# Optimization experiments

Measured on AMD Instinct MI355X. Metric: run time of the kernel, lower is better.

## Reference

```python
import jax, jax.numpy as jnp
import numpy as np

B, N = 2, 6
H, W = 64, 64            # BEV grid
FH, FW = 32, 88          # camera feature map
DIM, FEAT_DIM = 128, 128
HEADS, DH = 4, 32
QW1, QW2 = 8, 8          # query window
KW1, KW2 = 4, 11         # key/val window
IMG_H, IMG_W = 224, 480
EPS = 1e-5


def _ln(t, g, b):
    m = t.mean(-1, keepdims=True)
    v = ((t - m) ** 2).mean(-1, keepdims=True)
    return (t - m) / jnp.sqrt(v + EPS) * g + b


def _bn_relu_conv(t, g, b, Wc):
    # eval-mode BatchNorm2d (running_mean=0, running_var=1) -> ReLU -> 1x1 conv
    y = jax.nn.relu(t / jnp.sqrt(1.0 + EPS) * g[:, None, None] + b[:, None, None])
    return jnp.einsum('oc,nchw->nohw', Wc, y)


def _normalize(t, axis):
    n = jnp.sqrt(jnp.sum(t * t, axis=axis, keepdims=True))
    return t / jnp.maximum(n, 1e-12)


def _win(t, w1, w2):
    # (..., X*w1, Y*w2, d) -> (..., X, Y, w1, w2, d)
    s = t.shape
    t = t.reshape(*s[:-3], s[-3] // w1, w1, s[-2] // w2, w2, s[-1])
    return jnp.swapaxes(t, -4, -3)


def _unwin(t):
    # (..., X, Y, w1, w2, d) -> (..., X*w1, Y*w2, d)
    s = t.shape
    return jnp.swapaxes(t, -4, -3).reshape(*s[:-5], s[-5] * s[-3], s[-4] * s[-2], s[-1])


def _gridwin(t, w1, w2):
    bb, nn, Ht, Wt, d = t.shape
    t = t.reshape(bb, nn, w1, Ht // w1, w2, Wt // w2, d)
    return t.transpose(0, 1, 3, 5, 2, 4, 6)  # (b, n, X, Y, w1, w2, d)


def _cross_win_attn(qw, kw, vw, ln_g, ln_b, Wqkv, bqkv, Wp, bp, skip):
    b, n, X, Y, w1, w2, d = qw.shape
    f1, f2 = kw.shape[4], kw.shape[5]
    L = X * Y
    q = qw.transpose(0, 2, 3, 1, 4, 5, 6).reshape(b, L, n * w1 * w2, d)
    k = kw.transpose(0, 2, 3, 1, 4, 5, 6).reshape(b, L, n * f1 * f2, d)
    v = vw.transpose(0, 2, 3, 1, 4, 5, 6).reshape(b, L, n * f1 * f2, d)
    q = _ln(q, ln_g[0], ln_b[0]) @ Wqkv[0] + bqkv[0]
    k = _ln(k, ln_g[1], ln_b[1]) @ Wqkv[1] + bqkv[1]
    v = _ln(v, ln_g[2], ln_b[2]) @ Wqkv[2] + bqkv[2]
    split = lambda t: t.reshape(*t.shape[:-1], HEADS, DH)  # head-major channel split
    q, k, v = split(q), split(k), split(v)
    att = jax.nn.softmax(DH ** -0.5 * jnp.einsum('blqhd,blkhd->bhlqk', q, k), axis=-1)
    o = jnp.einsum('bhlqk,blkhd->blqhd', att, v).reshape(b, L, n * w1 * w2, HEADS * DH)
    o = o @ Wp + bp
    o = o.reshape(b, X, Y, n, w1, w2, d).mean(3)  # mean over cameras
    return o + skip


def _forward(x, grid, feature, I_inv, E_inv,
             bn_fl_g, bn_fl_b, W_fl, bn_fp_g, bn_fp_b, W_fp,
             W_bev, b_bev, W_img, W_cam,
             attn_ln_g, attn_ln_b, attn_Wqkv, attn_bqkv, attn_Wp, attn_bp,
             pn_g, pn_b, Wma, bma, Wmb, bmb, post_g, post_b):
    b, n = feature.shape[:2]
    # image plane (buffer)
    xs = jnp.linspace(0.0, 1.0, FW) * IMG_W
    ys = jnp.linspace(0.0, 1.0, FH) * IMG_H
    gx, gy = jnp.meshgrid(xs, ys)  # (FH, FW) each
    plane = jnp.stack([gx, gy, jnp.ones_like(gx)], 0).reshape(3, FH * FW)
    # camera embedding from translation column of E_inv
    c = E_inv[..., -1]                                   # (b, n, 4)
    c_embed = jnp.einsum('oc,bnc->bno', W_cam, c)        # (b, n, dim)
    # unprojected rays
    cam = jnp.einsum('bnij,jk->bnik', I_inv, plane)      # (b, n, 3, HW)
    cam = jnp.concatenate([cam, jnp.ones_like(cam[:, :, :1])], 2)
    d = jnp.einsum('bnij,bnjk->bnik', E_inv, cam)        # (b, n, 4, HW)
    d_img = d.reshape(b, n, 4, FH, FW)
    d_embed = jnp.einsum('oc,bnchw->bnohw', W_img, d_img)
    img_embed = _normalize(d_embed - c_embed[..., None, None], axis=2)
    # BEV positional embedding
    w_embed = jnp.einsum('oc,chw->ohw', W_bev, grid[:2]) + b_bev[:, None, None]
    bev_embed = _normalize(w_embed[None, None] - c_embed[..., None, None], axis=2)  # (b,n,dim,H,W)
    feat = feature.reshape(b * n, FEAT_DIM, FH, FW)
    key_im = img_embed + _bn_relu_conv(feat, bn_fp_g, bn_fp_b, W_fp).reshape(b, n, DIM, FH, FW)
    val_im = _bn_relu_conv(feat, bn_fl_g, bn_fl_b, W_fl).reshape(b, n, DIM, FH, FW)
    query = bev_embed + x[:, None]                       # (b, n, dim, H, W)
    # channel-last
    q_im = query.transpose(0, 1, 3, 4, 2)
    k_im = key_im.transpose(0, 1, 3, 4, 2)
    v_im = val_im.transpose(0, 1, 3, 4, 2)
    x_im = x.transpose(0, 2, 3, 1)
    # stage 1: local windows
    qw = _win(q_im, QW1, QW2)
    kw = _win(k_im, KW1, KW2)
    vw = _win(v_im, KW1, KW2)
    o1 = _cross_win_attn(qw, kw, vw, attn_ln_g[0], attn_ln_b[0], attn_Wqkv[0],
                         attn_bqkv[0], attn_Wp[0], attn_bp[0], _win(x_im, QW1, QW2))
    q1 = _unwin(o1)                                      # (b, H, W, d)
    q1 = q1 + jax.nn.gelu(_ln(q1, pn_g[0], pn_b[0]) @ Wma[0] + bma[0], approximate=False) @ Wmb[0] + bmb[0]
    # stage 2: grid (swapped) windows
    qg = jnp.broadcast_to(q1[:, None], (b, n) + q1.shape[1:])
    o2 = _cross_win_attn(_win(qg, QW1, QW2), _gridwin(k_im, KW1, KW2), _gridwin(v_im, KW1, KW2),
                         attn_ln_g[1], attn_ln_b[1], attn_Wqkv[1], attn_bqkv[1],
                         attn_Wp[1], attn_bp[1], _win(q1, QW1, QW2))
    q2 = _unwin(o2)
    q2 = q2 + jax.nn.gelu(_ln(q2, pn_g[1], pn_b[1]) @ Wma[1] + bma[1], approximate=False) @ Wmb[1] + bmb[1]
    out = _ln(q2, post_g, post_b)
    return out.transpose(0, 3, 1, 2)                     # (b, dim, H, W)


def setup_inputs() -> dict:
    key = jax.random.key(0)
    ks = jax.random.split(key, 16)
    rn = lambda i, shape, sc=0.02: jax.random.normal(ks[i], shape, dtype=jnp.float32) * sc
    return {
        'index': 0,
        'x': jax.random.normal(ks[0], (B, DIM, H, W), dtype=jnp.float32),
        'grid': jax.random.normal(ks[1], (2, H, W), dtype=jnp.float32),
        'feature': jax.random.normal(ks[2], (B, N, FEAT_DIM, FH, FW), dtype=jnp.float32),
        'I_inv': jax.random.normal(ks[3], (B, N, 3, 3), dtype=jnp.float32),
        'E_inv': jax.random.normal(ks[4], (B, N, 4, 4), dtype=jnp.float32),
        'bn_fl_g': jnp.ones((FEAT_DIM,), jnp.float32), 'bn_fl_b': jnp.zeros((FEAT_DIM,), jnp.float32),
        'W_fl': rn(5, (DIM, FEAT_DIM)),
        'bn_fp_g': jnp.ones((FEAT_DIM,), jnp.float32), 'bn_fp_b': jnp.zeros((FEAT_DIM,), jnp.float32),
        'W_fp': rn(6, (DIM, FEAT_DIM)),
        'W_bev': rn(7, (DIM, 2)), 'b_bev': jnp.zeros((DIM,), jnp.float32),
        'W_img': rn(8, (DIM, 4)), 'W_cam': rn(9, (DIM, 4)),
        'attn_ln_g': jnp.ones((2, 3, DIM), jnp.float32), 'attn_ln_b': jnp.zeros((2, 3, DIM), jnp.float32),
        'attn_Wqkv': rn(10, (2, 3, DIM, HEADS * DH)), 'attn_bqkv': jnp.zeros((2, 3, HEADS * DH), jnp.float32),
        'attn_Wp': rn(11, (2, HEADS * DH, DIM)), 'attn_bp': jnp.zeros((2, DIM), jnp.float32),
        'pn_g': jnp.ones((2, DIM), jnp.float32), 'pn_b': jnp.zeros((2, DIM), jnp.float32),
        'Wma': rn(12, (2, DIM, 2 * DIM)), 'bma': jnp.zeros((2, 2 * DIM), jnp.float32),
        'Wmb': rn(13, (2, 2 * DIM, DIM)), 'bmb': jnp.zeros((2, DIM), jnp.float32),
        'post_g': jnp.ones((DIM,), jnp.float32), 'post_b': jnp.zeros((DIM,), jnp.float32),
    }


def reference(index, x, grid, feature, I_inv, E_inv,
              bn_fl_g, bn_fl_b, W_fl, bn_fp_g, bn_fp_b, W_fp,
              W_bev, b_bev, W_img, W_cam,
              attn_ln_g, attn_ln_b, attn_Wqkv, attn_bqkv, attn_Wp, attn_bp,
              pn_g, pn_b, Wma, bma, Wmb, bmb, post_g, post_b):
    del index  # grid for this index is passed directly
    return _forward(x, grid, feature, I_inv, E_inv,
                    bn_fl_g, bn_fl_b, W_fl, bn_fp_g, bn_fp_b, W_fp,
                    W_bev, b_bev, W_img, W_cam,
                    attn_ln_g, attn_ln_b, attn_Wqkv, attn_bqkv, attn_Wp, attn_bp,
                    pn_g, pn_b, Wma, bma, Wmb, bmb, post_g, post_b)
```

## Files before the change

### kernel.cpp

```cpp
#include <hip/hip_runtime.h>
#include <math.h>


typedef __attribute__((ext_vector_type(8))) short short8;
typedef __attribute__((ext_vector_type(4))) float f32x4;

__device__ __forceinline__ unsigned short f2bf(float f){
  union { float f; unsigned u; } v; v.f = f;
  unsigned r = v.u + 0x7FFF + ((v.u >> 16) & 1);
  return (unsigned short)(r >> 16);
}
__device__ __forceinline__ float bf2f(unsigned short h){
  union { unsigned u; float f; } v; v.u = ((unsigned)h) << 16; return v.f;
}
__device__ __forceinline__ void store_bf16x8(unsigned short* p, const float* v){
  union { short8 s8; unsigned short u[8]; } u;
  #pragma unroll
  for (int i=0;i<8;i++) u.u[i] = f2bf(v[i]);
  *(short8*)p = u.s8;
}

__device__ __forceinline__ float gelu_erf(float x){
  float z = x * 0.70710678118654752f;
  float a = fabsf(z);
  float t = 1.0f / fmaf(0.3275911f, a, 1.0f);
  float p = t*(0.254829592f + t*(-0.284496736f + t*(1.421413741f +
            t*(-1.453152027f + t*1.061405429f))));
  float er = 1.0f - p*__expf(-a*a);
  er = copysignf(er, z);
  return 0.5f * x * (1.0f + er);
}

__device__ __forceinline__ size_t remap_kv(int tok, int mode){
  int bn = tok / 2816; int p = tok - bn*2816;
  int b = bn / 6, n = bn - b*6;
  int i = p / 88, j = p - i*88;
  int l, t;
  if (mode == 1){
    int jw = j / 11;
    l = (i >> 2)*8 + jw;
    t = n*44 + (i & 3)*11 + (j - jw*11);
  } else {
    l = (i & 7)*8 + (j & 7);
    t = n*44 + (i >> 3)*11 + (j >> 3);
  }
  return (size_t)((b*64 + l)*264 + t);
}

__global__ __launch_bounds__(256) void k_prepconv(
    const float* __restrict__ qkv, const float* __restrict__ wp,
    const float* __restrict__ wma, const float* __restrict__ wmb,
    unsigned short* __restrict__ Wt,
    const float* __restrict__ abqkv, float* __restrict__ biasP,
    const float* __restrict__ gridp, const float* __restrict__ Wbev,
    const float* __restrict__ bbev, const float* __restrict__ x,
    const float* __restrict__ lg, const float* __restrict__ lb,
    const float* __restrict__ Einv, const float* __restrict__ Wcam,
    unsigned short* __restrict__ QPh,
    const float* __restrict__ feat,
    const float* __restrict__ gfp, const float* __restrict__ bfp,
    const float* __restrict__ Wfp,
    const float* __restrict__ gfl, const float* __restrict__ bfl,
    const float* __restrict__ Wfl,
    const float* __restrict__ Iinv, const float* __restrict__ Wimg,
    unsigned short* __restrict__ K1h, unsigned short* __restrict__ V1h){
  constexpr int KP_ = 136;
  __shared__ unsigned short sW[128*KP_];
  __shared__ unsigned short sA[128*KP_];
  __shared__ __align__(16) float sMisc[2560];
  const int bid = blockIdx.x;
  const int tid = threadIdx.x;

  if (bid < 52){
    const int sel[13]  = {0,0,0,0,0, 1,1, 2,2, 3,3,3,3};
    const int soff[13] = {16384,32768,49152,65536,81920, 0,16384, 0,32768,
                          0,16384,32768,49152};
    const int doff[13] = {16384,32768,49152,65536,81920, 98304,114688,
                          131072,163840, 196608,212992,229376,245760};
    const int Ns[13]   = {128,128,128,128,128, 128,128, 256,256,
                          128,128,128,128};
    int sg = bid >> 2, q = bid & 3;
    const float* srcs[4] = {qkv, wp, wma, wmb};
    const float* src = srcs[sel[sg]] + soff[sg];
    unsigned short* dst = Wt + doff[sg];
    int K = 128, N = Ns[sg];
    int quarter = (K*N) >> 2;
    bool fold = (sg <= 4);
    const float* gv = lg + (sg+1)*128;
    for (int idx = q*quarter + tid; idx < (q+1)*quarter; idx += 256){
      int n = idx / K, k = idx - n*K;
      float v = src[k*N + n];
      if (fold) v *= gv[k];
      dst[idx] = f2bf(v);
    }
  } else if (bid < 58){
    if (tid < 128){
      int m = bid - 52;
      int n = tid;
      float s = abqkv[m*128 + n];
      if (m > 0){
        const float* lnb = lb + m*128;
        const float* W = qkv + m*16384;
        for (int k=0;k<128;k++) s = fmaf(lnb[k], W[k*128 + n], s);
      }
      biasP[m*128 + n] = s;
    }
  } else if (bid < 570){
    const float QSCALE = 0.17677669529663687f;
    float* sx = sMisc;
    int* rowoff = (int*)(sMisc + 2176);
    int bid2 = bid - 58;
    int b = bid2 >> 8; int pp0 = (bid2 & 255) << 4;
    for (int idx = tid; idx < 16384; idx += 256){
      int n = idx & 127, k = idx >> 7;
      sW[n*KP_ + k] = f2bf(qkv[(size_t)k*128 + n]);
    }
    {
      int cg = tid >> 4, px = tid & 15;
      #pragma unroll
      for (int i=0;i<8;i++){
        int c = cg + 16*i;
        sx[c*17 + px] = x[(size_t)b*524288 + (size_t)c*4096 + pp0 + px];
      }
    }
    if (tid < 16){
      int pix = pp0 + tid; int h = pix >> 6, w = pix & 63;
      int l = (h>>3)*8 + (w>>3); int tq = (h&7)*8 + (w&7);
      rowoff[tid] = (b*64 + l)*384 + tq;
    }
    __syncthreads();
    int xid = tid >> 4, part = tid & 15;
    int pix = pp0 + xid;
    float g0 = gridp[pix], g1 = gridp[4096 + pix];
    float we[8], xv[8];
    #pragma unroll
    for (int k=0;k<8;k++){
      int o = part*8 + k;
      we[k] = Wbev[o*2]*g0 + Wbev[o*2+1]*g1 + bbev[o];
      xv[k] = sx[(part*8+k)*17 + xid];
    }
    for (int n=0; n<6; n++){
      const float* E = Einv + (b*6+n)*16;
      float v[8]; float sq = 0.f;
      #pragma unroll
      for (int k=0;k<8;k++){
        int o = part*8 + k;
        const float* Wc = Wcam + o*4;
        float ce = Wc[0]*E[3] + Wc[1]*E[7] + Wc[2]*E[11] + Wc[3]*E[15];
        float vv = we[k] - ce;
        v[k] = vv; sq = fmaf(vv, vv, sq);
      }
      #pragma unroll
      for (int off=8; off>0; off>>=1) sq += __shfl_xor(sq, off, 16);
      float rn = 1.0f / fmaxf(sqrtf(sq), 1e-12f);
      float q[8]; float s=0.f, s2=0.f;
      #pragma unroll
      for (int k=0;k<8;k++){
        q[k] = fmaf(v[k], rn, xv[k]);
        s += q[k]; s2 = fmaf(q[k], q[k], s2);
      }
      #pragma unroll
      for (int off=8; off>0; off>>=1){ s += __shfl_xor(s, off, 16); s2 += __shfl_xor(s2, off, 16); }
      float mean = s*(1.f/128.f);
      float rstd = rsqrtf(fmaxf(s2*(1.f/128.f) - mean*mean, 0.f) + 1e-5f);
      float o8[8];
      #pragma unroll
      for (int k=0;k<8;k++){
        int c = part*8 + k;
        o8[k] = fmaf((q[k]-mean)*rstd, lg[c], lb[c]);
      }
      store_bf16x8(sA + (size_t)(n*16 + xid)*KP_ + part*8, o8);
    }
    __syncthreads();
    const int lane = tid & 63, wv = tid >> 6;
    const int lane15 = lane & 15, quad = lane >> 4;
    const int n0 = wv * 32;
    f32x4 acc[6][2];
    #pragma unroll
    for (int mt=0; mt<6; mt++){ acc[mt][0]=(f32x4)0.f; acc[mt][1]=(f32x4)0.f; }
    const unsigned short* aptr = sA + lane15*KP_ + quad*8;
    const unsigned short* bptr = sW + (size_t)(n0 + lane15)*KP_ + quad*8;
    #pragma unroll
    for (int kk=0; kk<4; kk++){
      short8 af[6], bf2v[2];
      #pragma unroll
      for (int mt=0; mt<6; mt++) af[mt] = *(const short8*)(aptr + mt*16*KP_ + kk*32);
      bf2v[0] = *(const short8*)(bptr + kk*32);
      bf2v[1] = *(const short8*)(bptr + 16*KP_ + kk*32);
      #pragma unroll
      for (int mt=0; mt<6; mt++){
        acc[mt][0] = __builtin_amdgcn_mfma_f32_16x16x32_bf16(af[mt], bf2v[0], acc[mt][0], 0,0,0);
        acc[mt][1] = __builtin_amdgcn_mfma_f32_16x16x32_bf16(af[mt], bf2v[1], acc[mt][1], 0,0,0);
      }
    }
    __syncthreads();
    #pragma unroll
    for (int nt=0; nt<2; nt++){
      int col = n0 + nt*16 + lane15;
      float bsv = abqkv[col];
      #pragma unroll
      for (int mt=0; mt<6; mt++){
        #pragma unroll
        for (int r4=0; r4<4; r4++){
          int row = mt*16 + quad*4 + r4;
          sA[row*KP_ + col] = f2bf((acc[mt][nt][r4] + bsv) * QSCALE);
        }
      }
    }
    __syncthreads();
    for (int i = tid; i < 1536; i += 256){
      int r = i >> 4, seg = i & 15;
      size_t grow = (size_t)rowoff[r & 15] + (r >> 4)*64;
      *(short8*)(QPh + grow*128 + seg*8) = *(const short8*)&sA[r*KP_ + seg*8];
    }
  } else {
    float* sg_  = sMisc;
    float* sb_  = sMisc + 128;
    float* sMean= sMisc + 256;
    float* sRstd= sMisc + 384;
    float* sRn  = sMisc + 512;
    float* sCE  = sMisc + 640;
    float4* sWI4= (float4*)(sMisc + 768);
    float* sIE  = sMisc + 1280;
    const int bid2c = bid - 570;
    const int which = (bid2c >= 264);
    const int cbid = which ? bid2c - 264 : bid2c;
    const float* gg = which ? gfl : gfp;
    const float* bb = which ? bfl : bfp;
    const float* Wf = which ? Wfl : Wfp;
    unsigned short* OUT = which ? V1h : K1h;
    const int base = cbid * 128;
    const int bn = base / 2816;
    const int pbase = base - bn*2816;
    for (int i = tid; i < 2048; i += 256){
      int n = i >> 4, k8 = (i & 15) << 3;
      const float* wsp = Wf + (size_t)n*128 + k8;
      float4 f0 = *(const float4*)wsp;
      float4 f1 = *(const float4*)(wsp+4);
      float v8[8] = {f0.x,f0.y,f0.z,f0.w,f1.x,f1.y,f1.z,f1.w};
      store_bf16x8(&sW[n*KP_ + k8], v8);
    }
    if (tid < 128){ sg_[tid]=gg[tid]; sb_[tid]=bb[tid]; }
    if (!which){
      if (tid < 128){
        const float* E = Einv + bn*16;
        float4 wc = *(const float4*)(Wcam + tid*4);
        sCE[tid] = wc.x*E[3] + wc.y*E[7] + wc.z*E[11] + wc.w*E[15];
        sWI4[tid] = *(const float4*)(Wimg + tid*4);
      }
      if (tid < 25) sIE[tid] = (tid < 9) ? Iinv[bn*9 + tid] : Einv[bn*16 + (tid-9)];
    }
    const float RSQ = rsqrtf(1.0f + 1e-5f);
    {
      int prow = tid & 127, cseg = tid >> 7;
      int p = pbase + prow;
      const float* fb = feat + ((size_t)bn*128 + cseg*64)*2816 + p;
      #pragma unroll 8
      for (int i=0;i<64;i+=2){
        int c = cseg*64 + i;
        float t0 = fb[(size_t)i*2816] * RSQ;
        float t1 = fb[(size_t)(i+1)*2816] * RSQ;
        float y0 = fmaxf(fmaf(t0, sg_[c],   sb_[c]),   0.f);
        float y1 = fmaxf(fmaf(t1, sg_[c+1], sb_[c+1]), 0.f);
        unsigned u = (unsigned)f2bf(y0) | ((unsigned)f2bf(y1) << 16);
        *(unsigned*)&sA[prow*KP_ + c] = u;
      }
    }
    __syncthreads();
    const int lane = tid & 63, wv = tid >> 6;
    const int lane15 = lane & 15, quad = lane >> 4;
    const int n0 = wv * 32;
    f32x4 acc[8][2];
    #pragma unroll
    for (int mt=0; mt<8; mt++){ acc[mt][0]=(f32x4)0.f; acc[mt][1]=(f32x4)0.f; }
    const unsigned short* aptr = sA + lane15*KP_ + quad*8;
    const unsigned short* bptr = sW + (size_t)(n0 + lane15)*KP_ + quad*8;
    #pragma unroll
    for (int kk=0; kk<4; kk++){
      short8 af[8], bf2v[2];
      #pragma unroll
      for (int mt=0; mt<8; mt++) af[mt] = *(const short8*)(aptr + mt*16*KP_ + kk*32);
      bf2v[0] = *(const short8*)(bptr + kk*32);
      bf2v[1] = *(const short8*)(bptr + 16*KP_ + kk*32);
      #pragma unroll
      for (int mt=0; mt<8; mt++){
        acc[mt][0] = __builtin_amdgcn_mfma_f32_16x16x32_bf16(af[mt], bf2v[0], acc[mt][0], 0,0,0);
        acc[mt][1] = __builtin_amdgcn_mfma_f32_16x16x32_bf16(af[mt], bf2v[1], acc[mt][1], 0,0,0);
      }
    }
    __syncthreads();
    if (!which){
      const int r = tid >> 1, half = tid & 1;
      int p = pbase + r;
      int ii = p / 88, jj = p - ii*88;
      float xs = (float)jj * (480.0f/87.0f);
      float ys = (float)ii * (224.0f/31.0f);
      float c0 = sIE[0]*xs + sIE[1]*ys + sIE[2];
      float c1 = sIE[3]*xs + sIE[4]*ys + sIE[5];
      float c2 = sIE[6]*xs + sIE[7]*ys + sIE[8];
      float d0 = sIE[9]*c0  + sIE[10]*c1 + sIE[11]*c2 + sIE[12];
      float d1 = sIE[13]*c0 + sIE[14]*c1 + sIE[15]*c2 + sIE[16];
      float d2 = sIE[17]*c0 + sIE[18]*c1 + sIE[19]*c2 + sIE[20];
      float d3 = sIE[21]*c0 + sIE[22]*c1 + sIE[23]*c2 + sIE[24];
      float sq = 0.f;
      #pragma unroll 8
      for (int k=0;k<64;k++){
        int c = half*64 + k;
        float4 w = sWI4[c];
        float de = w.x*d0 + w.y*d1 + w.z*d2 + w.w*d3 - sCE[c];
        sA[r*KP_ + c] = f2bf(de);
        sq = fmaf(de, de, sq);
      }
      sq += __shfl_xor(sq, 1);
      if (half == 0) sRn[r] = 1.0f / fmaxf(sqrtf(sq), 1e-12f);
    }
    __syncthreads();
    #pragma unroll
    for (int mt=0; mt<8; mt++){
      #pragma unroll
      for (int nt=0; nt<2; nt++){
        int col = n0 + nt*16 + lane15;
        #pragma unroll
        for (int r4=0; r4<4; r4++){
          int row = mt*16 + quad*4 + r4;
          float v = acc[mt][nt][r4];
          if (!which) v += bf2f(sA[row*KP_ + col]) * sRn[row];
          sA[row*KP_ + col] = f2bf(v);
        }
      }
    }
    __syncthreads();
    {
      int r = tid >> 1, part = tid & 1;
      float s=0.f, s2=0.f;
      #pragma unroll 8
      for (int k=0;k<64;k++){
        float v = bf2f(sA[r*KP_ + part*64 + k]);
        s += v; s2 = fmaf(v,v,s2);
      }
      s += __shfl_xor(s, 1); s2 += __shfl_xor(s2, 1);
      if (part == 0){
        float mean = s*(1.f/128.f);
        sMean[r] = mean;
        sRstd[r] = rsqrtf(fmaxf(s2*(1.f/128.f) - mean*mean, 0.f) + 1e-5f);
      }
    }
    __syncthreads();
    for (int i = tid; i < 2048; i += 256){
      int row = i >> 4, seg = i & 15;
      float mean = sMean[row], rstd = sRstd[row];
      union { short8 s; unsigned short u[8]; } t;
      t.s = *(const short8*)&sA[row*KP_ + seg*8];
      float v[8];
      #pragma unroll
      for (int k=0;k<8;k++) v[k] = (bf2f(t.u[k]) - mean)*rstd;
      store_bf16x8(OUT + (size_t)(base+row)*128 + seg*8, v);
    }
  }
}

__global__ __launch_bounds__(256) void k_kvdual(
    const unsigned short* __restrict__ K1h, const unsigned short* __restrict__ V1h,
    const unsigned short* __restrict__ WtK1, const unsigned short* __restrict__ WtK2,
    const unsigned short* __restrict__ WtV1, const unsigned short* __restrict__ WtV2,
    const float* __restrict__ biasP,
    unsigned short* __restrict__ KPh, unsigned short* __restrict__ KP2h,
    unsigned short* __restrict__ VPh, unsigned short* __restrict__ VP2h){
  constexpr int KP_ = 136;
  __shared__ unsigned short sW[128*KP_];
  __shared__ unsigned short sA[128*KP_];
  __shared__ float sbias[128];
  const int which = (blockIdx.x >= 264);
  const int cbid = which ? blockIdx.x - 264 : blockIdx.x;
  const int base = cbid * 128;
  const unsigned short* Xh = which ? V1h : K1h;
  const unsigned short* Wa = which ? WtV1 : WtK1;
  const unsigned short* Wb = which ? WtV2 : WtK2;
  unsigned short* Oa = which ? VPh : KPh;
  unsigned short* Ob = which ? VP2h : KP2h;
  const float* ba = biasP + (which ? 256 : 128);
  const float* bb = biasP + (which ? 640 : 512);
  const int tid = threadIdx.x;
  for (int i = tid; i < 2048; i += 256){
    int n = i >> 4, k8 = (i & 15) << 3;
    *(short8*)&sW[n*KP_ + k8] = *(const short8*)(Wa + (size_t)n*128 + k8);
  }
  {
    const int r = tid >> 1, part = tid & 1;
    const short8* src = (const short8*)(Xh + (size_t)(base+r)*128 + part*64);
    short8* dst = (short8*)(sA + r*KP_ + part*64);
    #pragma unroll
    for (int k=0;k<8;k++) dst[k] = src[k];
  }
  if (tid < 128) sbias[tid] = ba[tid];
  __syncthreads();
  const int lane = tid & 63, wv = tid >> 6;
  const int lane15 = lane & 15, quad = lane >> 4;
  const int n0 = wv * 32;
  const unsigned short* aptr = sA + lane15*KP_ + quad*8;
  const unsigned short* bptr = sW + (size_t)(n0 + lane15)*KP_ + quad*8;
  f32x4 acc[8][2];
  #pragma unroll
  for (int mt=0; mt<8; mt++){ acc[mt][0]=(f32x4)0.f; acc[mt][1]=(f32x4)0.f; }
  #pragma unroll
  for (int kk=0; kk<4; kk++){
    short8 af[8], bf2v[2];
    #pragma unroll
    for (int mt=0; mt<8; mt++) af[mt] = *(const short8*)(aptr + mt*16*KP_ + kk*32);
    bf2v[0] = *(const short8*)(bptr + kk*32);
    bf2v[1] = *(const short8*)(bptr + 16*KP_ + kk*32);
    #pragma unroll
    for (int mt=0; mt<8; mt++){
      acc[mt][0] = __builtin_amdgcn_mfma_f32_16x16x32_bf16(af[mt], bf2v[0], acc[mt][0], 0,0,0);
      acc[mt][1] = __builtin_amdgcn_mfma_f32_16x16x32_bf16(af[mt], bf2v[1], acc[mt][1], 0,0,0);
    }
  }
  __syncthreads();
  #pragma unroll
  for (int mt=0; mt<8; mt++){
    #pragma unroll
    for (int nt=0; nt<2; nt++){
      int col = n0 + nt*16 + lane15;
      float bsv = sbias[col];
      #pragma unroll
      for (int r4=0; r4<4; r4++){
        int row = mt*16 + quad*4 + r4;
        sW[row*KP_ + col] = f2bf(acc[mt][nt][r4] + bsv);
      }
    }
  }
  __syncthreads();
  for (int i = tid; i < 2048; i += 256){
    int row = i >> 4, seg = i & 15;
    size_t orow = remap_kv(base + row, 1);
    *(short8*)(Oa + orow*128 + seg*8) = *(const short8*)&sW[row*KP_ + seg*8];
  }
  if (tid < 128) sbias[tid] = bb[tid];
  __syncthreads();
  for (int i = tid; i < 2048; i += 256){
    int n = i >> 4, k8 = (i & 15) << 3;
    *(short8*)&sW[n*KP_ + k8] = *(const short8*)(Wb + (size_t)n*128 + k8);
  }
  __syncthreads();
  #pragma unroll
  for (int mt=0; mt<8; mt++){ acc[mt][0]=(f32x4)0.f; acc[mt][1]=(f32x4)0.f; }
  #pragma unroll
  for (int kk=0; kk<4; kk++){
    short8 af[8], bf2v[2];
    #pragma unroll
    for (int mt=0; mt<8; mt++) af[mt] = *(const short8*)(aptr + mt*16*KP_ + kk*32);
    bf2v[0] = *(const short8*)(bptr + kk*32);
    bf2v[1] = *(const short8*)(bptr + 16*KP_ + kk*32);
    #pragma unroll
    for (int mt=0; mt<8; mt++){
      acc[mt][0] = __builtin_amdgcn_mfma_f32_16x16x32_bf16(af[mt], bf2v[0], acc[mt][0], 0,0,0);
      acc[mt][1] = __builtin_amdgcn_mfma_f32_16x16x32_bf16(af[mt], bf2v[1], acc[mt][1], 0,0,0);
    }
  }
  __syncthreads();
  #pragma unroll
  for (int mt=0; mt<8; mt++){
    #pragma unroll
    for (int nt=0; nt<2; nt++){
      int col = n0 + nt*16 + lane15;
      float bsv = sbias[col];
      #pragma unroll
      for (int r4=0; r4<4; r4++){
        int row = mt*16 + quad*4 + r4;
        sA[row*KP_ + col] = f2bf(acc[mt][nt][r4] + bsv);
      }
    }
  }
  __syncthreads();
  for (int i = tid; i < 2048; i += 256){
    int row = i >> 4, seg = i & 15;
    size_t orow = remap_kv(base + row, 2);
    *(short8*)(Ob + orow*128 + seg*8) = *(const short8*)&sA[row*KP_ + seg*8];
  }
}

__global__ __launch_bounds__(256) void k_tail(
    const unsigned short* __restrict__ AOh,
    const float* __restrict__ skipf, int skipmode,
    const unsigned short* __restrict__ WtP, const float* __restrict__ abp,
    const float* __restrict__ png, const float* __restrict__ pnb,
    const unsigned short* __restrict__ WtMAa, const unsigned short* __restrict__ WtMAb,
    const float* __restrict__ bma,
    const unsigned short* __restrict__ WtMBa, const unsigned short* __restrict__ WtMBb,
    const float* __restrict__ bmb,
    float* __restrict__ Q1out,
    const unsigned short* __restrict__ WtQ2, const float* __restrict__ q2bias,
    float q2scale, unsigned short* __restrict__ QPout,
    const float* __restrict__ postg, const float* __restrict__ postb,
    float* __restrict__ out){
  constexpr int KP_ = 136;
  __shared__ unsigned short sW[128*KP_];
  __shared__ unsigned short sX[32*KP_];
  __shared__ unsigned short sH1[32*KP_];
  __shared__ unsigned short sH2[32*KP_];
  __shared__ float sCUR[32*132];
  __shared__ float sbias[128];
  __shared__ float sg[128], sb2[128];
  __shared__ float sMean[32], sRstd[32];
  const int tid = threadIdx.x;
  const int base = blockIdx.x * 32;
  const int lane = tid & 63, wv = tid >> 6;
  const int lane15 = lane & 15, quad = lane >> 4;
  const int n0 = wv * 32;

  auto loadW = [&](const unsigned short* Wp){
    for (int i = tid; i < 2048; i += 256){
      int n = i >> 4, k8 = (i & 15) << 3;
      *(short8*)&sW[n*KP_ + k8] = *(const short8*)(Wp + (size_t)n*128 + k8);
    }
  };
  auto domfma = [&](const unsigned short* Asrc, f32x4 acc[2][2]){
    const unsigned short* aptr = Asrc + lane15*KP_ + quad*8;
    const unsigned short* bptr = sW + (size_t)(n0 + lane15)*KP_ + quad*8;
    #pragma unroll
    for (int kk=0; kk<4; kk++){
      short8 a0 = *(const short8*)(aptr + kk*32);
      short8 a1 = *(const short8*)(aptr + 16*KP_ + kk*32);
      short8 b0 = *(const short8*)(bptr + kk*32);
      short8 b1 = *(const short8*)(bptr + 16*KP_ + kk*32);
      acc[0][0] = __builtin_amdgcn_mfma_f32_16x16x32_bf16(a0,b0,acc[0][0],0,0,0);
      acc[1][0] = __builtin_amdgcn_mfma_f32_16x16x32_bf16(a1,b0,acc[1][0],0,0,0);
      acc[0][1] = __builtin_amdgcn_mfma_f32_16x16x32_bf16(a0,b1,acc[0][1],0,0,0);
      acc[1][1] = __builtin_amdgcn_mfma_f32_16x16x32_bf16(a1,b1,acc[1][1],0,0,0);
    }
  };
// ... 336 lines not shown
  }
}

extern "C" void kernel_launch(void* const* d_in, const int* in_sizes, int n_in,
                              void* d_out, int out_size, void* d_ws, size_t ws_size,
                              hipStream_t stream) {
  (void)in_sizes; (void)n_in; (void)out_size; (void)ws_size;
  const float* x     = (const float*)d_in[1];
  const float* gridp = (const float*)d_in[2];
  const float* feat  = (const float*)d_in[3];
  const float* Iinv  = (const float*)d_in[4];
  const float* Einv  = (const float*)d_in[5];
  const float* gfl   = (const float*)d_in[6];
  const float* bfl   = (const float*)d_in[7];
  const float* Wfl   = (const float*)d_in[8];
  const float* gfp   = (const float*)d_in[9];
  const float* bfp   = (const float*)d_in[10];
  const float* Wfp   = (const float*)d_in[11];
  const float* Wbev  = (const float*)d_in[12];
  const float* bbev  = (const float*)d_in[13];
  const float* Wimg  = (const float*)d_in[14];
  const float* Wcam  = (const float*)d_in[15];
  const float* alng  = (const float*)d_in[16];
  const float* alnb  = (const float*)d_in[17];
  const float* aWqkv = (const float*)d_in[18];
  const float* abqkv = (const float*)d_in[19];
  const float* aWp   = (const float*)d_in[20];
  const float* abp   = (const float*)d_in[21];
  const float* png   = (const float*)d_in[22];
  const float* pnb   = (const float*)d_in[23];
  const float* Wma   = (const float*)d_in[24];
  const float* bma   = (const float*)d_in[25];
  const float* Wmb   = (const float*)d_in[26];
  const float* bmb   = (const float*)d_in[27];
  const float* postg = (const float*)d_in[28];
  const float* postb = (const float*)d_in[29];
  float* out = (float*)d_out;
  float* ws  = (float*)d_ws;
  const float QSC = 0.17677669529663687f;

  float* biasP = ws;
  unsigned short* Wt   = (unsigned short*)(ws + 2048);
  unsigned short* K1h  = (unsigned short*)(ws + 149504);
  unsigned short* V1h  = K1h + 4325376;
  unsigned short* KPh  = V1h + 4325376;
  unsigned short* VPh  = KPh + 4325376;
  unsigned short* KP2h = VPh + 4325376;
  unsigned short* VP2h = KP2h + 4325376;
  unsigned short* QPh  = VP2h + 4325376;
  unsigned short* Qbh  = QPh + 6291456;
  unsigned short* AOh  = Qbh + 6291456;
  float* Q1f = (float*)(AOh + 1048576);

  unsigned short* WtK1 = Wt + 16384;
  unsigned short* WtV1 = Wt + 32768;    unsigned short* WtQ2 = Wt + 49152;
  unsigned short* WtK2 = Wt + 65536;    unsigned short* WtV2 = Wt + 81920;
  unsigned short* WtP1 = Wt + 98304;    unsigned short* WtP2 = Wt + 114688;
  unsigned short* WtMA1 = Wt + 131072;  unsigned short* WtMA2 = Wt + 163840;
  unsigned short* WtMB1a = Wt + 196608; unsigned short* WtMB1b = Wt + 212992;
  unsigned short* WtMB2a = Wt + 229376; unsigned short* WtMB2b = Wt + 245760;

  k_prepconv<<<1098, 256, 0, stream>>>(aWqkv, aWp, Wma, Wmb, Wt,
      abqkv, biasP, gridp, Wbev, bbev, x, alng, alnb, Einv, Wcam, QPh,
      feat, gfp, bfp, Wfp, gfl, bfl, Wfl, Iinv, Wimg, K1h, V1h);

  k_kvdual<<<528, 256, 0, stream>>>(K1h, V1h, WtK1, WtK2, WtV1, WtV2,
      biasP, KPh, KP2h, VPh, VP2h);

  k_attn2<<<512, 256, 0, stream>>>(QPh, KPh, VPh, AOh, 6, 384);
  k_tail<<<256, 256, 0, stream>>>(AOh, x, 1, WtP1, abp, png, pnb,
      WtMA1, WtMA1+16384, bma, WtMB1a, WtMB1b, bmb, Q1f,
      WtQ2, biasP+384, QSC, QPh,
      nullptr, nullptr, nullptr);
  k_attn2<<<512, 256, 0, stream>>>(QPh, KP2h, VP2h, AOh, 1, 64);
  k_tail<<<256, 256, 0, stream>>>(AOh, Q1f, 3, WtP2, abp+128, png+128, pnb+128,
      WtMA2, WtMA2+16384, bma+256, WtMB2a, WtMB2b, bmb+128, nullptr,
      nullptr, nullptr, 0.f, nullptr,
      postg, postb, out);
}
```

Measured before the change: 255.8 us.

## Fuse K/V projection kernel into conv prep kernel, building weights per block

The separate k_kvdual launch is removed. Each conv block now keeps its normalized features in shared memory and runs both K/V projection GEMMs for stage 1 and stage 2 in place, avoiding the K1h/V1h round trip through global memory and one kernel launch. To break the dependency on the weight-prep blocks, every block rebuilds the LN-folded bf16 projection weights and projected biases from fp32 itself, which adds redundant per-block work. The long-running conv blocks are reordered to launch first, ahead of the Q and weight-prep blocks.

```diff
diff --git a/kernel.cpp b/kernel.cpp
--- a/kernel.cpp
+++ b/kernel.cpp
@@ -63,7 +63,8 @@
     const float* __restrict__ gfl, const float* __restrict__ bfl,
     const float* __restrict__ Wfl,
     const float* __restrict__ Iinv, const float* __restrict__ Wimg,
-    unsigned short* __restrict__ K1h, unsigned short* __restrict__ V1h){
+    unsigned short* __restrict__ KPh, unsigned short* __restrict__ KP2h,
+    unsigned short* __restrict__ VPh, unsigned short* __restrict__ VP2h){
   constexpr int KP_ = 136;
   __shared__ unsigned short sW[128*KP_];
   __shared__ unsigned short sA[128*KP_];
@@ -71,149 +72,7 @@
   const int bid = blockIdx.x;
   const int tid = threadIdx.x;
 
-  if (bid < 52){
-    const int sel[13]  = {0,0,0,0,0, 1,1, 2,2, 3,3,3,3};
-    const int soff[13] = {16384,32768,49152,65536,81920, 0,16384, 0,32768,
-                          0,16384,32768,49152};
-    const int doff[13] = {16384,32768,49152,65536,81920, 98304,114688,
-                          131072,163840, 196608,212992,229376,245760};
-    const int Ns[13]   = {128,128,128,128,128, 128,128, 256,256,
-                          128,128,128,128};
-    int sg = bid >> 2, q = bid & 3;
-    const float* srcs[4] = {qkv, wp, wma, wmb};
-    const float* src = srcs[sel[sg]] + soff[sg];
-    unsigned short* dst = Wt + doff[sg];
-    int K = 128, N = Ns[sg];
-    int quarter = (K*N) >> 2;
-    bool fold = (sg <= 4);
-    const float* gv = lg + (sg+1)*128;
-    for (int idx = q*quarter + tid; idx < (q+1)*quarter; idx += 256){
-      int n = idx / K, k = idx - n*K;
-      float v = src[k*N + n];
-      if (fold) v *= gv[k];
-      dst[idx] = f2bf(v);
-    }
-  } else if (bid < 58){
-    if (tid < 128){
-      int m = bid - 52;
-      int n = tid;
-      float s = abqkv[m*128 + n];
-      if (m > 0){
-        const float* lnb = lb + m*128;
-        const float* W = qkv + m*16384;
-        for (int k=0;k<128;k++) s = fmaf(lnb[k], W[k*128 + n], s);
-      }
-      biasP[m*128 + n] = s;
-    }
-  } else if (bid < 570){
-    const float QSCALE = 0.17677669529663687f;
-    float* sx = sMisc;
-    int* rowoff = (int*)(sMisc + 2176);
-    int bid2 = bid - 58;
-    int b = bid2 >> 8; int pp0 = (bid2 & 255) << 4;
-    for (int idx = tid; idx < 16384; idx += 256){
-      int n = idx & 127, k = idx >> 7;
-      sW[n*KP_ + k] = f2bf(qkv[(size_t)k*128 + n]);
-    }
-    {
-      int cg = tid >> 4, px = tid & 15;
-      #pragma unroll
-      for (int i=0;i<8;i++){
-        int c = cg + 16*i;
-        sx[c*17 + px] = x[(size_t)b*524288 + (size_t)c*4096 + pp0 + px];
-      }
-    }
-    if (tid < 16){
-      int pix = pp0 + tid; int h = pix >> 6, w = pix & 63;
-      int l = (h>>3)*8 + (w>>3); int tq = (h&7)*8 + (w&7);
-      rowoff[tid] = (b*64 + l)*384 + tq;
-    }
-    __syncthreads();
-    int xid = tid >> 4, part = tid & 15;
-    int pix = pp0 + xid;
-    float g0 = gridp[pix], g1 = gridp[4096 + pix];
-    float we[8], xv[8];
-    #pragma unroll
-    for (int k=0;k<8;k++){
-      int o = part*8 + k;
-      we[k] = Wbev[o*2]*g0 + Wbev[o*2+1]*g1 + bbev[o];
-      xv[k] = sx[(part*8+k)*17 + xid];
-    }
-    for (int n=0; n<6; n++){
-      const float* E = Einv + (b*6+n)*16;
-      float v[8]; float sq = 0.f;
-      #pragma unroll
-      for (int k=0;k<8;k++){
-        int o = part*8 + k;
-        const float* Wc = Wcam + o*4;
-        float ce = Wc[0]*E[3] + Wc[1]*E[7] + Wc[2]*E[11] + Wc[3]*E[15];
-        float vv = we[k] - ce;
-        v[k] = vv; sq = fmaf(vv, vv, sq);
-      }
-      #pragma unroll
-      for (int off=8; off>0; off>>=1) sq += __shfl_xor(sq, off, 16);
-      float rn = 1.0f / fmaxf(sqrtf(sq), 1e-12f);
-      float q[8]; float s=0.f, s2=0.f;
-      #pragma unroll
-      for (int k=0;k<8;k++){
-        q[k] = fmaf(v[k], rn, xv[k]);
-        s += q[k]; s2 = fmaf(q[k], q[k], s2);
-      }
-      #pragma unroll
-      for (int off=8; off>0; off>>=1){ s += __shfl_xor(s, off, 16); s2 += __shfl_xor(s2, off, 16); }
-      float mean = s*(1.f/128.f);
-      float rstd = rsqrtf(fmaxf(s2*(1.f/128.f) - mean*mean, 0.f) + 1e-5f);
-      float o8[8];
-      #pragma unroll
-      for (int k=0;k<8;k++){
-        int c = part*8 + k;
-        o8[k] = fmaf((q[k]-mean)*rstd, lg[c], lb[c]);
-      }
-      store_bf16x8(sA + (size_t)(n*16 + xid)*KP_ + part*8, o8);
-    }
-    __syncthreads();
-    const int lane = tid & 63, wv = tid >> 6;
-    const int lane15 = lane & 15, quad = lane >> 4;
-    const int n0 = wv * 32;
-    f32x4 acc[6][2];
-    #pragma unroll
-    for (int mt=0; mt<6; mt++){ acc[mt][0]=(f32x4)0.f; acc[mt][1]=(f32x4)0.f; }
-    const unsigned short* aptr = sA + lane15*KP_ + quad*8;
-    const unsigned short* bptr = sW + (size_t)(n0 + lane15)*KP_ + quad*8;
-    #pragma unroll
-    for (int kk=0; kk<4; kk++){
-      short8 af[6], bf2v[2];
-      #pragma unroll
-      for (int mt=0; mt<6; mt++) af[mt] = *(const short8*)(aptr + mt*16*KP_ + kk*32);
-      bf2v[0] = *(const short8*)(bptr + kk*32);
-      bf2v[1] = *(const short8*)(bptr + 16*KP_ + kk*32);
-      #pragma unroll
-      for (int mt=0; mt<6; mt++){
-        acc[mt][0] = __builtin_amdgcn_mfma_f32_16x16x32_bf16(af[mt], bf2v[0], acc[mt][0], 0,0,0);
-        acc[mt][1] = __builtin_amdgcn_mfma_f32_16x16x32_bf16(af[mt], bf2v[1], acc[mt][1], 0,0,0);
-      }
-    }
-    __syncthreads();
-    #pragma unroll
-    for (int nt=0; nt<2; nt++){
-      int col = n0 + nt*16 + lane15;
-      float bsv = abqkv[col];
-      #pragma unroll
-      for (int mt=0; mt<6; mt++){
-        #pragma unroll
-        for (int r4=0; r4<4; r4++){
-          int row = mt*16 + quad*4 + r4;
-          sA[row*KP_ + col] = f2bf((acc[mt][nt][r4] + bsv) * QSCALE);
-        }
-      }
-    }
-    __syncthreads();
-    for (int i = tid; i < 1536; i += 256){
-      int r = i >> 4, seg = i & 15;
-      size_t grow = (size_t)rowoff[r & 15] + (r >> 4)*64;
-      *(short8*)(QPh + grow*128 + seg*8) = *(const short8*)&sA[r*KP_ + seg*8];
-    }
-  } else {
+  if (bid < 528){
     float* sg_  = sMisc;
     float* sb_  = sMisc + 128;
     float* sMean= sMisc + 256;
@@ -222,16 +81,30 @@
     float* sCE  = sMisc + 640;
     float4* sWI4= (float4*)(sMisc + 768);
     float* sIE  = sMisc + 1280;
-    const int bid2c = bid - 570;
-    const int which = (bid2c >= 264);
-    const int cbid = which ? bid2c - 264 : bid2c;
+    float* sB1  = sMisc + 1312;
+    float* sB2  = sMisc + 1440;
+    const int which = (bid >= 264);
+    const int cbid = which ? bid - 264 : bid;
+    const int m1 = which ? 2 : 1;
+    const int m2 = which ? 5 : 4;
     const float* gg = which ? gfl : gfp;
     const float* bb = which ? bfl : bfp;
     const float* Wf = which ? Wfl : Wfp;
-    unsigned short* OUT = which ? V1h : K1h;
+    unsigned short* Oa = which ? VPh : KPh;
+    unsigned short* Ob = which ? VP2h : KP2h;
     const int base = cbid * 128;
     const int bn = base / 2816;
     const int pbase = base - bn*2816;
+    if (tid < 128){ sg_[tid]=gg[tid]; sb_[tid]=bb[tid]; }
+    if (!which){
+      if (tid < 128){
+        const float* E = Einv + bn*16;
+        float4 wc = *(const float4*)(Wcam + tid*4);
+        sCE[tid] = wc.x*E[3] + wc.y*E[7] + wc.z*E[11] + wc.w*E[15];
+        sWI4[tid] = *(const float4*)(Wimg + tid*4);
+      }
+      if (tid < 25) sIE[tid] = (tid < 9) ? Iinv[bn*9 + tid] : Einv[bn*16 + (tid-9)];
+    }
     for (int i = tid; i < 2048; i += 256){
       int n = i >> 4, k8 = (i & 15) << 3;
       const float* wsp = Wf + (size_t)n*128 + k8;
@@ -240,15 +113,14 @@
       float v8[8] = {f0.x,f0.y,f0.z,f0.w,f1.x,f1.y,f1.z,f1.w};
       store_bf16x8(&sW[n*KP_ + k8], v8);
     }
-    if (tid < 128){ sg_[tid]=gg[tid]; sb_[tid]=bb[tid]; }
-    if (!which){
-      if (tid < 128){
-        const float* E = Einv + bn*16;
-        float4 wc = *(const float4*)(Wcam + tid*4);
-        sCE[tid] = wc.x*E[3] + wc.y*E[7] + wc.z*E[11] + wc.w*E[15];
-        sWI4[tid] = *(const float4*)(Wimg + tid*4);
-      }
-      if (tid < 25) sIE[tid] = (tid < 9) ? Iinv[bn*9 + tid] : Einv[bn*16 + (tid-9)];
+    {
+      int n = tid & 127, wsel = tid >> 7;
+      int m = wsel ? m2 : m1;
+      const float* W = qkv + m*16384;
+      const float* lnb = lb + m*128;
+      float s = abqkv[m*128 + n];
+      for (int k=0;k<128;k++) s = fmaf(lnb[k], W[k*128 + n], s);
+      (wsel ? sB2 : sB1)[n] = s;
     }
     const float RSQ = rsqrtf(1.0f + 1e-5f);
     {
@@ -270,11 +142,11 @@
     const int lane = tid & 63, wv = tid >> 6;
     const int lane15 = lane & 15, quad = lane >> 4;
     const int n0 = wv * 32;
-    f32x4 acc[8][2];
-    #pragma unroll
-    for (int mt=0; mt<8; mt++){ acc[mt][0]=(f32x4)0.f; acc[mt][1]=(f32x4)0.f; }
     const unsigned short* aptr = sA + lane15*KP_ + quad*8;
     const unsigned short* bptr = sW + (size_t)(n0 + lane15)*KP_ + quad*8;
+    f32x4 acc[8][2];
+    #pragma unroll
+    for (int mt=0; mt<8; mt++){ acc[mt][0]=(f32x4)0.f; acc[mt][1]=(f32x4)0.f; }
     #pragma unroll
     for (int kk=0; kk<4; kk++){
       short8 af[8], bf2v[2];
@@ -314,6 +186,16 @@
       sq += __shfl_xor(sq, 1);
       if (half == 0) sRn[r] = 1.0f / fmaxf(sqrtf(sq), 1e-12f);
     }
+    {
+      const float* Wsrc = qkv + m1*16384;
+      const float* gvv = lg + m1*128;
+      for (int idx = tid; idx < 8192; idx += 256){
+        int n = idx & 127, k2 = (idx >> 7) << 1;
+        float v0 = Wsrc[(size_t)k2*128 + n]     * gvv[k2];
+        float v1 = Wsrc[(size_t)(k2+1)*128 + n] * gvv[k2+1];
+        *(unsigned*)&sW[n*KP_ + k2] = (unsigned)f2bf(v0) | ((unsigned)f2bf(v1) << 16);
+      }
+    }
     __syncthreads();
     #pragma unroll
     for (int mt=0; mt<8; mt++){
@@ -354,128 +236,229 @@
       float v[8];
       #pragma unroll
       for (int k=0;k<8;k++) v[k] = (bf2f(t.u[k]) - mean)*rstd;
-      store_bf16x8(OUT + (size_t)(base+row)*128 + seg*8, v);
-    }
-  }
-}
-
-__global__ __launch_bounds__(256) void k_kvdual(
-    const unsigned short* __restrict__ K1h, const unsigned short* __restrict__ V1h,
-    const unsigned short* __restrict__ WtK1, const unsigned short* __restrict__ WtK2,
-    const unsigned short* __restrict__ WtV1, const unsigned short* __restrict__ WtV2,
-    const float* __restrict__ biasP,
-    unsigned short* __restrict__ KPh, unsigned short* __restrict__ KP2h,
-    unsigned short* __restrict__ VPh, unsigned short* __restrict__ VP2h){
-  constexpr int KP_ = 136;
-  __shared__ unsigned short sW[128*KP_];
-  __shared__ unsigned short sA[128*KP_];
-  __shared__ float sbias[128];
-  const int which = (blockIdx.x >= 264);
-  const int cbid = which ? blockIdx.x - 264 : blockIdx.x;
-  const int base = cbid * 128;
-  const unsigned short* Xh = which ? V1h : K1h;
-  const unsigned short* Wa = which ? WtV1 : WtK1;
-  const unsigned short* Wb = which ? WtV2 : WtK2;
-  unsigned short* Oa = which ? VPh : KPh;
-  unsigned short* Ob = which ? VP2h : KP2h;
-  const float* ba = biasP + (which ? 256 : 128);
-  const float* bb = biasP + (which ? 640 : 512);
-  const int tid = threadIdx.x;
-  for (int i = tid; i < 2048; i += 256){
-    int n = i >> 4, k8 = (i & 15) << 3;
-    *(short8*)&sW[n*KP_ + k8] = *(const short8*)(Wa + (size_t)n*128 + k8);
-  }
-  {
-    const int r = tid >> 1, part = tid & 1;
-    const short8* src = (const short8*)(Xh + (size_t)(base+r)*128 + part*64);
-    short8* dst = (short8*)(sA + r*KP_ + part*64);
-    #pragma unroll
-    for (int k=0;k<8;k++) dst[k] = src[k];
-  }
-  if (tid < 128) sbias[tid] = ba[tid];
-  __syncthreads();
-  const int lane = tid & 63, wv = tid >> 6;
-  const int lane15 = lane & 15, quad = lane >> 4;
-  const int n0 = wv * 32;
-  const unsigned short* aptr = sA + lane15*KP_ + quad*8;
-  const unsigned short* bptr = sW + (size_t)(n0 + lane15)*KP_ + quad*8;
-  f32x4 acc[8][2];
-  #pragma unroll
-  for (int mt=0; mt<8; mt++){ acc[mt][0]=(f32x4)0.f; acc[mt][1]=(f32x4)0.f; }
-  #pragma unroll
-  for (int kk=0; kk<4; kk++){
-    short8 af[8], bf2v[2];
-    #pragma unroll
-    for (int mt=0; mt<8; mt++) af[mt] = *(const short8*)(aptr + mt*16*KP_ + kk*32);
-    bf2v[0] = *(const short8*)(bptr + kk*32);
-    bf2v[1] = *(const short8*)(bptr + 16*KP_ + kk*32);
+      store_bf16x8(&sA[row*KP_ + seg*8], v);
+    }
+    __syncthreads();
+    #pragma unroll
+    for (int mt=0; mt<8; mt++){ acc[mt][0]=(f32x4)0.f; acc[mt][1]=(f32x4)0.f; }
+    #pragma unroll
+    for (int kk=0; kk<4; kk++){
+      short8 af[8], bf2v[2];
+      #pragma unroll
+      for (int mt=0; mt<8; mt++) af[mt] = *(const short8*)(aptr + mt*16*KP_ + kk*32);
+      bf2v[0] = *(const short8*)(bptr + kk*32);
+      bf2v[1] = *(const short8*)(bptr + 16*KP_ + kk*32);
+      #pragma unroll
+      for (int mt=0; mt<8; mt++){
+        acc[mt][0] = __builtin_amdgcn_mfma_f32_16x16x32_bf16(af[mt], bf2v[0], acc[mt][0], 0,0,0);
+        acc[mt][1] = __builtin_amdgcn_mfma_f32_16x16x32_bf16(af[mt], bf2v[1], acc[mt][1], 0,0,0);
+      }
+    }
+    __syncthreads();
     #pragma unroll
     for (int mt=0; mt<8; mt++){
-      acc[mt][0] = __builtin_amdgcn_mfma_f32_16x16x32_bf16(af[mt], bf2v[0], acc[mt][0], 0,0,0);
-      acc[mt][1] = __builtin_amdgcn_mfma_f32_16x16x32_bf16(af[mt], bf2v[1], acc[mt][1], 0,0,0);
-    }
-  }
-  __syncthreads();
-  #pragma unroll
-  for (int mt=0; mt<8; mt++){
+      #pragma unroll
+      for (int nt=0; nt<2; nt++){
+        int col = n0 + nt*16 + lane15;
+        float bsv = sB1[col];
+        #pragma unroll
+        for (int r4=0; r4<4; r4++){
+          int row = mt*16 + quad*4 + r4;
+          sW[row*KP_ + col] = f2bf(acc[mt][nt][r4] + bsv);
+        }
+      }
+    }
+    __syncthreads();
+    for (int i = tid; i < 2048; i += 256){
+      int row = i >> 4, seg = i & 15;
+      size_t orow = remap_kv(base + row, 1);
+      *(short8*)(Oa + orow*128 + seg*8) = *(const short8*)&sW[row*KP_ + seg*8];
+    }
+    __syncthreads();
+    {
+      const float* Wsrc = qkv + m2*16384;
+      const float* gvv = lg + m2*128;
+      for (int idx = tid; idx < 8192; idx += 256){
+        int n = idx & 127, k2 = (idx >> 7) << 1;
+        float v0 = Wsrc[(size_t)k2*128 + n]     * gvv[k2];
+        float v1 = Wsrc[(size_t)(k2+1)*128 + n] * gvv[k2+1];
+        *(unsigned*)&sW[n*KP_ + k2] = (unsigned)f2bf(v0) | ((unsigned)f2bf(v1) << 16);
+      }
+    }
+    __syncthreads();
+    #pragma unroll
+    for (int mt=0; mt<8; mt++){ acc[mt][0]=(f32x4)0.f; acc[mt][1]=(f32x4)0.f; }
+    #pragma unroll
+    for (int kk=0; kk<4; kk++){
+      short8 af[8], bf2v[2];
+      #pragma unroll
+      for (int mt=0; mt<8; mt++) af[mt] = *(const short8*)(aptr + mt*16*KP_ + kk*32);
+      bf2v[0] = *(const short8*)(bptr + kk*32);
+      bf2v[1] = *(const short8*)(bptr + 16*KP_ + kk*32);
+      #pragma unroll
+      for (int mt=0; mt<8; mt++){
+        acc[mt][0] = __builtin_amdgcn_mfma_f32_16x16x32_bf16(af[mt], bf2v[0], acc[mt][0], 0,0,0);
+        acc[mt][1] = __builtin_amdgcn_mfma_f32_16x16x32_bf16(af[mt], bf2v[1], acc[mt][1], 0,0,0);
+      }
+    }
+    __syncthreads();
+    #pragma unroll
+    for (int mt=0; mt<8; mt++){
+      #pragma unroll
+      for (int nt=0; nt<2; nt++){
+        int col = n0 + nt*16 + lane15;
+        float bsv = sB2[col];
+        #pragma unroll
+        for (int r4=0; r4<4; r4++){
+          int row = mt*16 + quad*4 + r4;
+          sA[row*KP_ + col] = f2bf(acc[mt][nt][r4] + bsv);
+        }
+      }
+    }
+    __syncthreads();
+    for (int i = tid; i < 2048; i += 256){
+      int row = i >> 4, seg = i & 15;
+      size_t orow = remap_kv(base + row, 2);
+      *(short8*)(Ob + orow*128 + seg*8) = *(const short8*)&sA[row*KP_ + seg*8];
+    }
+  } else if (bid < 1040){
+    const float QSCALE = 0.17677669529663687f;
+    float* sx = sMisc;
+    int* rowoff = (int*)(sMisc + 2176);
+    int bid2 = bid - 528;
+    int b = bid2 >> 8; int pp0 = (bid2 & 255) << 4;
+    for (int idx = tid; idx < 16384; idx += 256){
+      int n = idx & 127, k = idx >> 7;
+      sW[n*KP_ + k] = f2bf(qkv[(size_t)k*128 + n]);
+    }
+    {
+      int cg = tid >> 4, px = tid & 15;
+      #pragma unroll
+      for (int i=0;i<8;i++){
+        int c = cg + 16*i;
+        sx[c*17 + px] = x[(size_t)b*524288 + (size_t)c*4096 + pp0 + px];
+      }
+    }
+    if (tid < 16){
+      int pix = pp0 + tid; int h = pix >> 6, w = pix & 63;
+      int l = (h>>3)*8 + (w>>3); int tq = (h&7)*8 + (w&7);
+      rowoff[tid] = (b*64 + l)*384 + tq;
+    }
+    __syncthreads();
+    int xid = tid >> 4, part = tid & 15;
+    int pix = pp0 + xid;
+    float g0 = gridp[pix], g1 = gridp[4096 + pix];
+    float we[8], xv[8];
+    #pragma unroll
+    for (int k=0;k<8;k++){
+      int o = part*8 + k;
+      we[k] = Wbev[o*2]*g0 + Wbev[o*2+1]*g1 + bbev[o];
+      xv[k] = sx[(part*8+k)*17 + xid];
+    }
+    for (int n=0; n<6; n++){
+      const float* E = Einv + (b*6+n)*16;
+      float v[8]; float sq = 0.f;
+      #pragma unroll
+      for (int k=0;k<8;k++){
+        int o = part*8 + k;
+        const float* Wc = Wcam + o*4;
+        float ce = Wc[0]*E[3] + Wc[1]*E[7] + Wc[2]*E[11] + Wc[3]*E[15];
+        float vv = we[k] - ce;
+        v[k] = vv; sq = fmaf(vv, vv, sq);
+      }
+      #pragma unroll
+      for (int off=8; off>0; off>>=1) sq += __shfl_xor(sq, off, 16);
+      float rn = 1.0f / fmaxf(sqrtf(sq), 1e-12f);
+      float q[8]; float s=0.f, s2=0.f;
+      #pragma unroll
+      for (int k=0;k<8;k++){
+        q[k] = fmaf(v[k], rn, xv[k]);
+        s += q[k]; s2 = fmaf(q[k], q[k], s2);
+      }
+      #pragma unroll
+      for (int off=8; off>0; off>>=1){ s += __shfl_xor(s, off, 16); s2 += __shfl_xor(s2, off, 16); }
+      float mean = s*(1.f/128.f);
+      float rstd = rsqrtf(fmaxf(s2*(1.f/128.f) - mean*mean, 0.f) + 1e-5f);
+      float o8[8];
+      #pragma unroll
+      for (int k=0;k<8;k++){
+        int c = part*8 + k;
+        o8[k] = fmaf((q[k]-mean)*rstd, lg[c], lb[c]);
+      }
+      store_bf16x8(sA + (size_t)(n*16 + xid)*KP_ + part*8, o8);
+    }
+    __syncthreads();
+    const int lane = tid & 63, wv = tid >> 6;
+    const int lane15 = lane & 15, quad = lane >> 4;
+    const int n0 = wv * 32;
+    f32x4 acc[6][2];
+    #pragma unroll
+    for (int mt=0; mt<6; mt++){ acc[mt][0]=(f32x4)0.f; acc[mt][1]=(f32x4)0.f; }
+    const unsigned short* aptr = sA + lane15*KP_ + quad*8;
+    const unsigned short* bptr = sW + (size_t)(n0 + lane15)*KP_ + quad*8;
+    #pragma unroll
+    for (int kk=0; kk<4; kk++){
+      short8 af[6], bf2v[2];
+      #pragma unroll
+      for (int mt=0; mt<6; mt++) af[mt] = *(const short8*)(aptr + mt*16*KP_ + kk*32);
+      bf2v[0] = *(const short8*)(bptr + kk*32);
+      bf2v[1] = *(const short8*)(bptr + 16*KP_ + kk*32);
+      #pragma unroll
+      for (int mt=0; mt<6; mt++){
+        acc[mt][0] = __builtin_amdgcn_mfma_f32_16x16x32_bf16(af[mt], bf2v[0], acc[mt][0], 0,0,0);
+        acc[mt][1] = __builtin_amdgcn_mfma_f32_16x16x32_bf16(af[mt], bf2v[1], acc[mt][1], 0,0,0);
+      }
+    }
+    __syncthreads();
     #pragma unroll
     for (int nt=0; nt<2; nt++){
       int col = n0 + nt*16 + lane15;
-      float bsv = sbias[col];
-      #pragma unroll
-      for (int r4=0; r4<4; r4++){
-        int row = mt*16 + quad*4 + r4;
-        sW[row*KP_ + col] = f2bf(acc[mt][nt][r4] + bsv);
-      }
-    }
-  }
-  __syncthreads();
-  for (int i = tid; i < 2048; i += 256){
-    int row = i >> 4, seg = i & 15;
-    size_t orow = remap_kv(base + row, 1);
-    *(short8*)(Oa + orow*128 + seg*8) = *(const short8*)&sW[row*KP_ + seg*8];
-  }
-  if (tid < 128) sbias[tid] = bb[tid];
-  __syncthreads();
-  for (int i = tid; i < 2048; i += 256){
-    int n = i >> 4, k8 = (i & 15) << 3;
-    *(short8*)&sW[n*KP_ + k8] = *(const short8*)(Wb + (size_t)n*128 + k8);
-  }
-  __syncthreads();
-  #pragma unroll
-  for (int mt=0; mt<8; mt++){ acc[mt][0]=(f32x4)0.f; acc[mt][1]=(f32x4)0.f; }
-  #pragma unroll
-  for (int kk=0; kk<4; kk++){
-    short8 af[8], bf2v[2];
-    #pragma unroll
-    for (int mt=0; mt<8; mt++) af[mt] = *(const short8*)(aptr + mt*16*KP_ + kk*32);
-    bf2v[0] = *(const short8*)(bptr + kk*32);
-    bf2v[1] = *(const short8*)(bptr + 16*KP_ + kk*32);
-    #pragma unroll
-    for (int mt=0; mt<8; mt++){
-      acc[mt][0] = __builtin_amdgcn_mfma_f32_16x16x32_bf16(af[mt], bf2v[0], acc[mt][0], 0,0,0);
-      acc[mt][1] = __builtin_amdgcn_mfma_f32_16x16x32_bf16(af[mt], bf2v[1], acc[mt][1], 0,0,0);
-    }
-  }
-  __syncthreads();
-  #pragma unroll
-  for (int mt=0; mt<8; mt++){
-    #pragma unroll
-    for (int nt=0; nt<2; nt++){
-      int col = n0 + nt*16 + lane15;
-      float bsv = sbias[col];
-      #pragma unroll
-      for (int r4=0; r4<4; r4++){
-        int row = mt*16 + quad*4 + r4;
-        sA[row*KP_ + col] = f2bf(acc[mt][nt][r4] + bsv);
-      }
-    }
-  }
-  __syncthreads();
-  for (int i = tid; i < 2048; i += 256){
-    int row = i >> 4, seg = i & 15;
-    size_t orow = remap_kv(base + row, 2);
-    *(short8*)(Ob + orow*128 + seg*8) = *(const short8*)&sA[row*KP_ + seg*8];
+      float bsv = abqkv[col];
+      #pragma unroll
+      for (int mt=0; mt<6; mt++){
+        #pragma unroll
+        for (int r4=0; r4<4; r4++){
+          int row = mt*16 + quad*4 + r4;
+          sA[row*KP_ + col] = f2bf((acc[mt][nt][r4] + bsv) * QSCALE);
+        }
+      }
+    }
+    __syncthreads();
+    for (int i = tid; i < 1536; i += 256){
+      int r = i >> 4, seg = i & 15;
+      size_t grow = (size_t)rowoff[r & 15] + (r >> 4)*64;
+      *(short8*)(QPh + grow*128 + seg*8) = *(const short8*)&sA[r*KP_ + seg*8];
+    }
+  } else if (bid < 1076){
+    const int sel[9]  = {0, 1,1, 2,2, 3,3,3,3};
+    const int soff[9] = {49152, 0,16384, 0,32768, 0,16384,32768,49152};
+    const int doff[9] = {49152, 98304,114688, 131072,163840,
+                         196608,212992,229376,245760};
+    const int Ns[9]   = {128, 128,128, 256,256, 128,128,128,128};
+    int bidw = bid - 1040;
+    int sg = bidw >> 2, q = bidw & 3;
+    const float* srcs[4] = {qkv, wp, wma, wmb};
+    const float* src = srcs[sel[sg]] + soff[sg];
+    unsigned short* dst = Wt + doff[sg];
+    int K = 128, N = Ns[sg];
+    int quarter = (K*N) >> 2;
+    bool fold = (sg == 0);
+    const float* gv = lg + 384;
+    for (int idx = q*quarter + tid; idx < (q+1)*quarter; idx += 256){
+      int n = idx / K, k = idx - n*K;
+      float v = src[k*N + n];
+      if (fold) v *= gv[k];
+      dst[idx] = f2bf(v);
+    }
+  } else {
+    if (tid < 128){
+      int n = tid;
+      const float* lnb = lb + 384;
+      const float* W = qkv + 49152;
+      float s = abqkv[384 + n];
+      for (int k=0;k<128;k++) s = fmaf(lnb[k], W[k*128 + n], s);
+      biasP[384 + n] = s;
+    }
   }
 }
 
@@ -918,20 +901,16 @@
   unsigned short* AOh  = Qbh + 6291456;
   float* Q1f = (float*)(AOh + 1048576);
 
-  unsigned short* WtK1 = Wt + 16384;
-  unsigned short* WtV1 = Wt + 32768;    unsigned short* WtQ2 = Wt + 49152;
-  unsigned short* WtK2 = Wt + 65536;    unsigned short* WtV2 = Wt + 81920;
+  unsigned short* WtQ2 = Wt + 49152;
   unsigned short* WtP1 = Wt + 98304;    unsigned short* WtP2 = Wt + 114688;
   unsigned short* WtMA1 = Wt + 131072;  unsigned short* WtMA2 = Wt + 163840;
   unsigned short* WtMB1a = Wt + 196608; unsigned short* WtMB1b = Wt + 212992;
   unsigned short* WtMB2a = Wt + 229376; unsigned short* WtMB2b = Wt + 245760;
 
-  k_prepconv<<<1098, 256, 0, stream>>>(aWqkv, aWp, Wma, Wmb, Wt,
+  k_prepconv<<<1077, 256, 0, stream>>>(aWqkv, aWp, Wma, Wmb, Wt,
       abqkv, biasP, gridp, Wbev, bbev, x, alng, alnb, Einv, Wcam, QPh,
-      feat, gfp, bfp, Wfp, gfl, bfl, Wfl, Iinv, Wimg, K1h, V1h);
-
-  k_kvdual<<<528, 256, 0, stream>>>(K1h, V1h, WtK1, WtK2, WtV1, WtV2,
-      biasP, KPh, KP2h, VPh, VP2h);
+      feat, gfp, bfp, Wfp, gfl, bfl, Wfl, Iinv, Wimg,
+      KPh, KP2h, VPh, VP2h);
 
   k_attn2<<<512, 256, 0, stream>>>(QPh, KPh, VPh, AOh, 6, 384);
   k_tail<<<256, 256, 0, stream>>>(AOh, x, 1, WtP1, abp, png, pnb,
```

Result: no change. 252.5 us (-1.3%).
